# Kernel optimization log

Hardware: AMD Instinct MI355X
Metric: run time of the kernel (lower is better)

## Reference

```python
import jax, jax.numpy as jnp
import numpy as np

EMBED_DIM = 384
NUM_HEADS = 6
HEAD_DIM = EMBED_DIM // NUM_HEADS
MLP_HIDDEN = 4 * EMBED_DIM
LN_EPS = 1e-5


def layer_norm(x, gamma, beta):
    mu = jnp.mean(x, axis=-1, keepdims=True)
    var = jnp.mean((x - mu) ** 2, axis=-1, keepdims=True)
    return (x - mu) * jax.lax.rsqrt(var + LN_EPS) * gamma + beta


def setup_inputs() -> dict:
    key = jax.random.key(0)
    ks = jax.random.split(key, 8)
    D, H = EMBED_DIM, MLP_HIDDEN
    s = 1.0 / np.sqrt(D)
    sh = 1.0 / np.sqrt(H)
    return {
        "x": jax.random.normal(ks[0], (16, 1024, D), dtype=jnp.float32),
        "ln1_g": jnp.ones((D,), jnp.float32),
        "ln1_b": jnp.zeros((D,), jnp.float32),
        "qkv_w": jax.random.uniform(ks[1], (3 * D, D), jnp.float32, -s, s),
        "qkv_b": jax.random.uniform(ks[2], (3 * D,), jnp.float32, -s, s),
        "proj_w": jax.random.uniform(ks[3], (D, D), jnp.float32, -s, s),
        "proj_b": jax.random.uniform(ks[4], (D,), jnp.float32, -s, s),
        "ln2_g": jnp.ones((D,), jnp.float32),
        "ln2_b": jnp.zeros((D,), jnp.float32),
        "fc1_w": jax.random.uniform(ks[5], (H, D), jnp.float32, -s, s),
        "fc1_b": jax.random.uniform(ks[6], (H,), jnp.float32, -s, s),
        "fc2_w": jax.random.uniform(ks[7], (D, H), jnp.float32, -sh, sh),
        "fc2_b": jnp.zeros((D,), jnp.float32),
    }


def reference(x, ln1_g, ln1_b, qkv_w, qkv_b, proj_w, proj_b,
              ln2_g, ln2_b, fc1_w, fc1_b, fc2_w, fc2_b):
    B, N, D = x.shape
    Hh, Dh = NUM_HEADS, HEAD_DIM
    scale = Dh ** -0.5

    # --- attention sublayer (pre-norm) ---
    h = layer_norm(x, ln1_g, ln1_b)
    qkv = h @ qkv_w.T + qkv_b                      # [B,N,3D]
    qkv = qkv.reshape(B, N, 3, Hh, Dh)
    q, k, v = (qkv[:, :, i].transpose(0, 2, 1, 3) for i in range(3))  # [B,H,N,Dh]
    attn = jax.nn.softmax(jnp.einsum('bhnd,bhmd->bhnm', q, k) * scale, axis=-1)
    o = jnp.einsum('bhnm,bhmd->bhnd', attn, v)     # [B,H,N,Dh]
    o = o.transpose(0, 2, 1, 3).reshape(B, N, D)
    x = x + (o @ proj_w.T + proj_b)

    # --- MLP sublayer (pre-norm) ---
    h = layer_norm(x, ln2_g, ln2_b)
    h = jax.nn.gelu(h @ fc1_w.T + fc1_b, approximate=False)
    x = x + (h @ fc2_w.T + fc2_b)
    return x
```

## Files before the change

kernel.cpp:

```cpp
#include <hip/hip_runtime.h>

typedef unsigned short u16;
typedef unsigned int   u32;
typedef __bf16  bf16x8 __attribute__((ext_vector_type(8)));
typedef __bf16  bf16x4_t __attribute__((ext_vector_type(4)));
typedef float   f32x4  __attribute__((ext_vector_type(4)));
typedef float   f32x2  __attribute__((ext_vector_type(2)));

struct Ptrs { const void* p[13]; };

extern "C" __device__ float __ocml_native_exp2_f32(float);

__device__ __forceinline__ float bf2f(u16 u) {
    union { unsigned int i; float f; } c; c.i = ((unsigned int)u) << 16; return c.f;
}
__device__ __forceinline__ u16 f2bf(float f) {
    union { float f; unsigned int i; } c; c.f = f;
    unsigned int u = c.i;
    unsigned int r = (u + 0x7fffu + ((u >> 16) & 1u)) >> 16;
    return (u16)r;
}

__device__ __forceinline__ float wave_sum(float x) {
#pragma unroll
    for (int m = 32; m >= 1; m >>= 1) x += __shfl_xor(x, m);
    return x;
}

__device__ __forceinline__ void g2l16(const u16* g, u16* l) {
    __builtin_amdgcn_global_load_lds(
        (__attribute__((address_space(1))) void*)g,
        (__attribute__((address_space(3))) void*)l, 16, 0, 0);
}

__device__ __forceinline__ int sniff_bf16(const u32* __restrict__ w) {
    int cnt = 0;
    for (int i = 0; i < 32; ++i) {
        u16 lo = (u16)(w[i] & 0xFFFFu);
        int e = (lo >> 7) & 0xFF;
        cnt += (e >= 117 && e <= 123) ? 1 : 0;
    }
    return (cnt >= 16) ? 1 : 0;
}

__global__ __launch_bounds__(256) void k_cvt_ln1(Ptrs ps,
                                                 u16* __restrict__ cw,
                                                 int* __restrict__ flagp,
                                                 u16* __restrict__ cx,
                                                 u16* __restrict__ h)
{
    const int flag = sniff_bf16((const u32*)ps.p[3]);
    if (blockIdx.x == 0 && threadIdx.x == 0) *flagp = flag;

    if (blockIdx.x < 867) {
        const int cum[13] = {0,48,96,55392,55536,73968,74016,74064,74112,
                             147840,148032,221760,221808};
        const int off[12] = {0,384,768,443136,444288,591744,
                             592128,592512,592896,1182720,1184256,1774080};
        int c = blockIdx.x * 256 + threadIdx.x;
        if (c >= 221808) return;
        int seg = 0;
#pragma unroll
        for (int i = 1; i < 12; ++i) seg += (c >= cum[i]) ? 1 : 0;
        int e = (c - cum[seg]) * 8;
        u16* dst = cw + off[seg] + e;
        if (flag) {
            *(uint4*)dst = *((const uint4*)ps.p[seg + 1] + (e >> 3));
        } else {
            const float* s = (const float*)ps.p[seg + 1] + e;
            u16 tmp[8];
#pragma unroll
            for (int t = 0; t < 8; ++t) tmp[t] = f2bf(s[t]);
            *(uint4*)dst = *(const uint4*)tmp;
        }
        return;
    }

    const int wid = threadIdx.x >> 6, lane = threadIdx.x & 63;
    const int row = (blockIdx.x - 867) * 4 + wid;
    const int e0 = lane * 6;
    float v[6]; u16 raw[6];
    float gv[6], bv[6];
    if (flag) {
        const u16* p = (const u16*)ps.p[0] + (size_t)row * 384 + e0;
        u32 w0 = *(const u32*)(p);
        u32 w1 = *(const u32*)(p + 2);
        u32 w2 = *(const u32*)(p + 4);
        raw[0] = (u16)w0; raw[1] = (u16)(w0 >> 16);
        raw[2] = (u16)w1; raw[3] = (u16)(w1 >> 16);
        raw[4] = (u16)w2; raw[5] = (u16)(w2 >> 16);
#pragma unroll
        for (int t = 0; t < 6; t++) v[t] = bf2f(raw[t]);
        const u16* gp = (const u16*)ps.p[1] + e0;
        const u16* bp = (const u16*)ps.p[2] + e0;
#pragma unroll
        for (int t = 0; t < 6; t++) { gv[t] = bf2f(gp[t]); bv[t] = bf2f(bp[t]); }
    } else {
        const float* p = (const float*)ps.p[0] + (size_t)row * 384 + e0;
        f32x2 a0 = *(const f32x2*)(p);
        f32x2 a1 = *(const f32x2*)(p + 2);
        f32x2 a2 = *(const f32x2*)(p + 4);
        v[0] = a0[0]; v[1] = a0[1]; v[2] = a1[0];
        v[3] = a1[1]; v[4] = a2[0]; v[5] = a2[1];
#pragma unroll
        for (int t = 0; t < 6; t++) raw[t] = f2bf(v[t]);
        const float* gp = (const float*)ps.p[1] + e0;
        const float* bp = (const float*)ps.p[2] + e0;
#pragma unroll
        for (int t = 0; t < 6; t++) { gv[t] = gp[t]; bv[t] = bp[t]; }
    }
    u32* pc = (u32*)(cx + (size_t)row * 384 + e0);
    pc[0] = (u32)raw[0] | ((u32)raw[1] << 16);
    pc[1] = (u32)raw[2] | ((u32)raw[3] << 16);
    pc[2] = (u32)raw[4] | ((u32)raw[5] << 16);
    float s = 0.f;
#pragma unroll
    for (int t = 0; t < 6; t++) s += v[t];
    const float mu = wave_sum(s) * (1.0f / 384.0f);
    float vs = 0.f;
#pragma unroll
    for (int t = 0; t < 6; t++) { float d = v[t] - mu; vs += d * d; }
    const float var = wave_sum(vs) * (1.0f / 384.0f);
    const float rs = rsqrtf(var + 1e-5f);
    u16 ow[6];
#pragma unroll
    for (int t = 0; t < 6; t++)
        ow[t] = f2bf((v[t] - mu) * rs * gv[t] + bv[t]);
    u32* po = (u32*)(h + (size_t)row * 384 + e0);
    po[0] = (u32)ow[0] | ((u32)ow[1] << 16);
    po[1] = (u32)ow[2] | ((u32)ow[3] << 16);
    po[2] = (u32)ow[4] | ((u32)ow[5] << 16);
}

template <bool SWAP = false>
__device__ __forceinline__ void gemm_core_128(const u16* __restrict__ A,
                                              const u16* __restrict__ B,
                                              int K, int m0, int n0,
                                              f32x4 (&acc)[4][4])
{
    __shared__ __align__(16) u16 As[128 * 64];
    __shared__ __align__(16) u16 Bs[128 * 64];

    const int tid  = threadIdx.x;
    const int lane = tid & 63;
    const int wid  = tid >> 6;
    const int wm  = (wid >> 1) * 64;
    const int wn  = (wid & 1) * 64;
    const int l15 = lane & 15;
    const int g   = lane >> 4;
    const int srow   = lane >> 3;
    const int schunk = ((lane & 7) ^ srow) * 8;

    const u16* Abase = A + (size_t)(m0 + wid * 32 + srow) * K + schunk;
    const u16* Bbase = B + (size_t)(n0 + wid * 32 + srow) * K + schunk;

    for (int kk = 0; kk < K; kk += 64) {
        __syncthreads();
#pragma unroll
        for (int t = 0; t < 4; ++t) {
            g2l16(Abase + (size_t)t * 8 * K + kk, &As[(wid * 32 + t * 8) * 64]);
            g2l16(Bbase + (size_t)t * 8 * K + kk, &Bs[(wid * 32 + t * 8) * 64]);
        }
        __syncthreads();

#pragma unroll
        for (int ks = 0; ks < 2; ++ks) {
            bf16x8 af[4], bfr[4];
#pragma unroll
            for (int i = 0; i < 4; i++) {
                int row = wm + 16 * i + l15;
                int p = ((ks * 4 + g) ^ (l15 & 7)) * 8;
                af[i] = __builtin_bit_cast(bf16x8,
                         *(const uint4*)&As[row * 64 + p]);
            }
#pragma unroll
            for (int j = 0; j < 4; j++) {
                int row = wn + 16 * j + l15;
                int p = ((ks * 4 + g) ^ (l15 & 7)) * 8;
                bfr[j] = __builtin_bit_cast(bf16x8,
                         *(const uint4*)&Bs[row * 64 + p]);
            }
#pragma unroll
            for (int i = 0; i < 4; i++)
#pragma unroll
                for (int j = 0; j < 4; j++) {
                    if (SWAP)
                        acc[i][j] = __builtin_amdgcn_mfma_f32_16x16x32_bf16(
                                        bfr[j], af[i], acc[i][j], 0, 0, 0);
                    else
                        acc[i][j] = __builtin_amdgcn_mfma_f32_16x16x32_bf16(
                                        af[i], bfr[j], acc[i][j], 0, 0, 0);
                }
        }
    }
}

__device__ __forceinline__ void gemm_core_128x64(const u16* __restrict__ A,
                                                 const u16* __restrict__ B,
                                                 int K, int m0, int n0,
                                                 f32x4 (&acc)[4][2])
{
    __shared__ __align__(16) u16 As[128 * 64];
    __shared__ __align__(16) u16 Bs[64 * 64];

    const int tid  = threadIdx.x;
    const int lane = tid & 63;
    const int wid  = tid >> 6;
    const int wm  = (wid >> 1) * 64;
    const int wn  = (wid & 1) * 32;
    const int l15 = lane & 15;
    const int g   = lane >> 4;
    const int srow   = lane >> 3;
    const int schunk = ((lane & 7) ^ srow) * 8;

    const u16* Abase = A + (size_t)(m0 + wid * 32 + srow) * K + schunk;
    const u16* Bbase = B + (size_t)(n0 + wid * 16 + srow) * K + schunk;

    for (int kk = 0; kk < K; kk += 64) {
        __syncthreads();
#pragma unroll
        for (int t = 0; t < 4; ++t)
            g2l16(Abase + (size_t)t * 8 * K + kk, &As[(wid * 32 + t * 8) * 64]);
#pragma unroll
        for (int t = 0; t < 2; ++t)
            g2l16(Bbase + (size_t)t * 8 * K + kk, &Bs[(wid * 16 + t * 8) * 64]);
        __syncthreads();

#pragma unroll
        for (int ks = 0; ks < 2; ++ks) {
            bf16x8 af[4], bfr[2];
#pragma unroll
            for (int i = 0; i < 4; i++) {
                int row = wm + 16 * i + l15;
                int p = ((ks * 4 + g) ^ (l15 & 7)) * 8;
                af[i] = __builtin_bit_cast(bf16x8,
                         *(const uint4*)&As[row * 64 + p]);
            }
#pragma unroll
            for (int j = 0; j < 2; j++) {
                int row = wn + 16 * j + l15;
                int p = ((ks * 4 + g) ^ (l15 & 7)) * 8;
                bfr[j] = __builtin_bit_cast(bf16x8,
                         *(const uint4*)&Bs[row * 64 + p]);
            }
#pragma unroll
            for (int i = 0; i < 4; i++)
#pragma unroll
                for (int j = 0; j < 2; j++)
                    acc[i][j] = __builtin_amdgcn_mfma_f32_16x16x32_bf16(
                                    af[i], bfr[j], acc[i][j], 0, 0, 0);
        }
    }
}

__global__ __launch_bounds__(256) void k_layernorm(const u16* __restrict__ in,
                                                   const u16* __restrict__ g,
                                                   const u16* __restrict__ b,
                                                   u16* __restrict__ out,
                                                   int nrows)
{
    const int wid = threadIdx.x >> 6, lane = threadIdx.x & 63;
    const int row = blockIdx.x * 4 + wid;
    if (row >= nrows) return;
    const int e0 = lane * 6;
    float v[6];
    const u16* p = in + (size_t)row * 384 + e0;
    u32 w0 = *(const u32*)(p);
    u32 w1 = *(const u32*)(p + 2);
    u32 w2 = *(const u32*)(p + 4);
    v[0] = bf2f((u16)w0); v[1] = bf2f((u16)(w0 >> 16));
    v[2] = bf2f((u16)w1); v[3] = bf2f((u16)(w1 >> 16));
    v[4] = bf2f((u16)w2); v[5] = bf2f((u16)(w2 >> 16));
    float s = 0.f;
#pragma unroll
    for (int t = 0; t < 6; t++) s += v[t];
    const float mu = wave_sum(s) * (1.0f / 384.0f);
    float vs = 0.f;
#pragma unroll
    for (int t = 0; t < 6; t++) { float d = v[t] - mu; vs += d * d; }
    const float var = wave_sum(vs) * (1.0f / 384.0f);
    const float rs = rsqrtf(var + 1e-5f);
    const u32* gg = (const u32*)(g + e0);
    const u32* bb = (const u32*)(b + e0);
    u32 gw[3] = {gg[0], gg[1], gg[2]};
    u32 bw[3] = {bb[0], bb[1], bb[2]};
    u16 ow[6];
#pragma unroll
    for (int t = 0; t < 6; t++) {
        u16 ge = (u16)(gw[t >> 1] >> ((t & 1) * 16));
        u16 be = (u16)(bw[t >> 1] >> ((t & 1) * 16));
        ow[t] = f2bf((v[t] - mu) * rs * bf2f(ge) + bf2f(be));
    }
    u32* po = (u32*)(out + (size_t)row * 384 + e0);
    po[0] = (u32)ow[0] | ((u32)ow[1] << 16);
    po[1] = (u32)ow[2] | ((u32)ow[3] << 16);
    po[2] = (u32)ow[4] | ((u32)ow[5] << 16);
}

__global__ __launch_bounds__(256) void k_gemm_qkv(const u16* __restrict__ A,
                                                  const u16* __restrict__ W,
                                                  const u16* __restrict__ bias,
                                                  u16* __restrict__ q,
                                                  u16* __restrict__ kbuf,
                                                  u16* __restrict__ vT)
{
    const int id = blockIdx.x, slot = id & 7, idx = id >> 3;
    const int m0 = (slot * 16 + idx / 9) * 128;
    const int n0 = (idx % 9) * 128;
    f32x4 acc[4][4];
#pragma unroll
    for (int i = 0; i < 4; i++)
#pragma unroll
        for (int j = 0; j < 4; j++) acc[i][j] = f32x4{0.f, 0.f, 0.f, 0.f};
    gemm_core_128<true>(A, W, 384, m0, n0, acc);
    const int lane = threadIdx.x & 63, wid = threadIdx.x >> 6;
    const int wm = (wid >> 1) * 64, wn = (wid & 1) * 64;
    const int l15 = lane & 15, rq = (lane >> 4) * 4;
#pragma unroll
    for (int i = 0; i < 4; i++) {
        const int gr = m0 + wm + 16 * i + l15;
        const int bb = gr >> 10, nn = gr & 1023;
#pragma unroll
        for (int j = 0; j < 4; j++) {
            const int gcb = n0 + wn + 16 * j + rq;
            const int part = gcb / 384, rem = gcb % 384;
            const int head = rem >> 6, dhb = rem & 63;
            const int bh = bb * 6 + head;
            float vals[4];
#pragma unroll
            for (int r = 0; r < 4; r++) vals[r] = acc[i][j][r] + bf2f(bias[gcb + r]);
            if (part == 2) {
#pragma unroll
                for (int r = 0; r < 4; r++)
                    vT[((size_t)bh * 64 + dhb + r) * 1024 + nn] = f2bf(vals[r]);
            } else {
                u16* dst = part ? kbuf : q;
                u32 lo = (u32)f2bf(vals[0]) | ((u32)f2bf(vals[1]) << 16);
                u32 hi = (u32)f2bf(vals[2]) | ((u32)f2bf(vals[3]) << 16);
                uint2 pk; pk.x = lo; pk.y = hi;
                *(uint2*)&dst[((size_t)bh * 1024 + nn) * 64 + dhb] = pk;
            }
        }
    }
}

__global__ __launch_bounds__(256) void k_attn(const u16* __restrict__ q,
                                              const u16* __restrict__ kk,
                                              const u16* __restrict__ vT,
                                              u16* __restrict__ o)
{
    __shared__ __align__(16) u16 Ks[128 * 64];
    __shared__ __align__(16) u16 Vs[2][64 * 64];
    __shared__ __align__(16) u16 Ps[128 * 64];

    const int tid = threadIdx.x, lane = tid & 63, wid = tid >> 6;
    const int l15 = lane & 15, g = lane >> 4, q8 = g * 8;
    const int id = blockIdx.x;
    const int bh = (id & 7) * 12 + ((id >> 3) >> 3);
    const int q0 = ((id >> 3) & 7) * 128;
    const int wrow = wid * 32;

    const u16* Q = q  + (size_t)bh * 65536;
    const u16* K = kk + (size_t)bh * 65536;
    const u16* V = vT + (size_t)bh * 65536;

    const int srow   = lane >> 3;
    const int schunk = ((lane & 7) ^ srow) * 8;
    const int rd0 = ((0 + g) ^ (l15 & 7)) * 8;
    const int rd1 = ((4 + g) ^ (l15 & 7)) * 8;
    int pcol[4];
#pragma unroll
    for (int ip = 0; ip < 4; ++ip)
        pcol[ip] = (((ip * 2 + (g >> 1)) ^ (l15 & 7)) * 8) + (g & 1) * 4;

    bf16x8 aq[2][2];
#pragma unroll
    for (int jp = 0; jp < 2; ++jp)
#pragma unroll
        for (int ks = 0; ks < 2; ++ks) {
            bf16x8 t = __builtin_bit_cast(bf16x8,
                *(const uint4*)&Q[(size_t)(q0 + wrow + jp * 16 + l15) * 64
                                  + ks * 32 + q8]);
#pragma unroll
            for (int e = 0; e < 8; ++e)
                t[e] = (__bf16)((float)t[e] * 0.18033688f);
            aq[jp][ks] = t;
        }

    f32x4 ob[2][4];
#pragma unroll
    for (int i = 0; i < 2; ++i)
#pragma unroll
        for (int j = 0; j < 4; ++j) ob[i][j] = f32x4{0.f, 0.f, 0.f, 0.f};
    float lsum[2] = {0.f, 0.f};

    for (int kt2 = 0; kt2 < 8; ++kt2) {
        __syncthreads();
#pragma unroll
        for (int t = 0; t < 4; ++t) {
            int r0 = wid * 32 + t * 8;
            g2l16(&K[(size_t)(kt2 * 128 + r0 + srow) * 64 + schunk], &Ks[r0 * 64]);
        }
#pragma unroll
        for (int h = 0; h < 2; ++h)
#pragma unroll
            for (int t = 0; t < 2; ++t) {
                int r0 = wid * 16 + t * 8;
                g2l16(&V[(size_t)(r0 + srow) * 1024 + kt2 * 128 + h * 64 + schunk],
                      &Vs[h][r0 * 64]);
            }
        __syncthreads();

#pragma unroll 1
        for (int h = 0; h < 2; ++h) {
            f32x4 st[4][2];
#pragma unroll
            for (int ip = 0; ip < 4; ++ip)
#pragma unroll
                for (int jp = 0; jp < 2; ++jp) st[ip][jp] = f32x4{0.f,0.f,0.f,0.f};
            __builtin_amdgcn_s_setprio(1);
#pragma unroll
            for (int ip = 0; ip < 4; ++ip) {
                int rbase = (h * 64 + ip * 16 + l15) * 64;
                bf16x8 bk0 = __builtin_bit_cast(bf16x8,
                    *(const uint4*)&Ks[rbase + rd0]);
                bf16x8 bk1 = __builtin_bit_cast(bf16x8,
                    *(const uint4*)&Ks[rbase + rd1]);
#pragma unroll
                for (int jp = 0; jp < 2; ++jp) {
                    st[ip][jp] = __builtin_amdgcn_mfma_f32_16x16x32_bf16(
                                    bk0, aq[jp][0], st[ip][jp], 0, 0, 0);
                    st[ip][jp] = __builtin_amdgcn_mfma_f32_16x16x32_bf16(
                                    bk1, aq[jp][1], st[ip][jp], 0, 0, 0);
                }
            }
            __builtin_amdgcn_s_setprio(0);

#pragma unroll
            for (int jp = 0; jp < 2; ++jp) {
                float ps = 0.f;
#pragma unroll
                for (int ip = 0; ip < 4; ++ip)
#pragma unroll
                    for (int r = 0; r < 4; ++r) {
                        float p = __ocml_native_exp2_f32(st[ip][jp][r]);
                        st[ip][jp][r] = p;
                        ps += p;
                    }
                lsum[jp] += ps;
            }

#pragma unroll
            for (int ip = 0; ip < 4; ++ip)
#pragma unroll
                for (int jp = 0; jp < 2; ++jp) {
                    bf16x4_t pk;
#pragma unroll
                    for (int r = 0; r < 4; ++r) pk[r] = (__bf16)st[ip][jp][r];
                    *(bf16x4_t*)&Ps[(wrow + jp*16 + l15) * 64 + pcol[ip]] = pk;
                }

            __builtin_amdgcn_s_setprio(1);
#pragma unroll
            for (int ks = 0; ks < 2; ++ks) {
                const int rdo = ks ? rd1 : rd0;
                bf16x8 ap[2];
#pragma unroll
                for (int i = 0; i < 2; ++i)
                    ap[i] = __builtin_bit_cast(bf16x8,
                        *(const uint4*)&Ps[(wrow + i*16 + l15) * 64 + rdo]);
#pragma unroll
                for (int jv = 0; jv < 4; ++jv) {
                    bf16x8 bv = __builtin_bit_cast(bf16x8,
                        *(const uint4*)&Vs[h][(jv * 16 + l15) * 64 + rdo]);
#pragma unroll
                    for (int i = 0; i < 2; ++i)
                        ob[i][jv] = __builtin_amdgcn_mfma_f32_16x16x32_bf16(
                                      ap[i], bv, ob[i][jv], 0, 0, 0);
                }
            }
            __builtin_amdgcn_s_setprio(0);
        }
    }

#pragma unroll
    for (int jp = 0; jp < 2; ++jp) {
        lsum[jp] += __shfl_xor(lsum[jp], 16);
        lsum[jp] += __shfl_xor(lsum[jp], 32);
    }
    const int bb = bh / 6, hh = bh % 6;
#pragma unroll
    for (int i = 0; i < 2; ++i)
#pragma unroll
        for (int r = 0; r < 4; ++r) {
            int src = (lane & 48) | (g * 4 + r);
            float linv = 1.0f / __shfl(lsum[i], src);
            int row = q0 + wrow + i * 16 + g * 4 + r;
#pragma unroll
            for (int jv = 0; jv < 4; ++jv) {
                int dh = jv * 16 + l15;
                o[((size_t)(bb * 1024 + row)) * 384 + hh * 64 + dh] =
                    f2bf(ob[i][jv][r] * linv);
            }
        }
}

__global__ __launch_bounds__(256) void k_gemm_proj(const u16* __restrict__ A,
                                                   const u16* __restrict__ W,
                                                   const u16* __restrict__ bias,
                                                   const u16* __restrict__ xin,
                                                   u16* __restrict__ x1)
{
    const int id = blockIdx.x, slot = id & 7, idx = id >> 3;
    const int m0 = (slot * 16 + idx / 6) * 128;
    const int n0 = (idx % 6) * 64;
    f32x4 acc[4][2];
#pragma unroll
    for (int i = 0; i < 4; i++)
#pragma unroll
        for (int j = 0; j < 2; j++) acc[i][j] = f32x4{0.f, 0.f, 0.f, 0.f};
    gemm_core_128x64(A, W, 384, m0, n0, acc);
    const int lane = threadIdx.x & 63, wid = threadIdx.x >> 6;
    const int wm = (wid >> 1) * 64, wn = (wid & 1) * 32;
    const int l15 = lane & 15, rq = (lane >> 4) * 4;
#pragma unroll
    for (int i = 0; i < 4; i++)
#pragma unroll
        for (int j = 0; j < 2; j++)
#pragma unroll
            for (int r = 0; r < 4; r++) {
                int gr = m0 + wm + 16 * i + rq + r;
                int gc = n0 + wn + 16 * j + l15;
                size_t ix = (size_t)gr * 384 + gc;
                x1[ix] = f2bf(acc[i][j][r] + bf2f(bias[gc]) + bf2f(xin[ix]));
            }
}

__global__ __launch_bounds__(256) void k_gemm_fc1(const u16* __restrict__ A,
                                                  const u16* __restrict__ W,
                                                  const u16* __restrict__ bias,
                                                  u16* __restrict__ hmid)
{
    const int id = blockIdx.x, slot = id & 7, idx = id >> 3;
    const int mbase = (slot * 8 + idx / 12) * 256;
    const int n0 = (idx % 12) * 128;
#pragma unroll 1
    for (int sub = 0; sub < 2; ++sub) {
        const int m0 = mbase + sub * 128;
        f32x4 acc[4][4];
#pragma unroll
        for (int i = 0; i < 4; i++)
#pragma unroll
            for (int j = 0; j < 4; j++) acc[i][j] = f32x4{0.f, 0.f, 0.f, 0.f};
        gemm_core_128(A, W, 384, m0, n0, acc);
        const int lane = threadIdx.x & 63, wid = threadIdx.x >> 6;
        const int wm = (wid >> 1) * 64, wn = (wid & 1) * 64;
        const int l15 = lane & 15, rq = (lane >> 4) * 4;
#pragma unroll
        for (int i = 0; i < 4; i++)
#pragma unroll
            for (int j = 0; j < 4; j++)
#pragma unroll
                for (int r = 0; r < 4; r++) {
                    int gr = m0 + wm + 16 * i + rq + r;
                    int gc = n0 + wn + 16 * j + l15;
                    float v = acc[i][j][r] + bf2f(bias[gc]);
                    float u2 = v * (2.3022084f + 0.1029433f * v * v);
                    float ge = v * __builtin_amdgcn_rcpf(
                                   1.0f + __ocml_native_exp2_f32(-u2));
                    hmid[(size_t)gr * 1536 + gc] = f2bf(ge);
                }
    }
}

__global__ __launch_bounds__(256) void k_gemm_fc2(const u16* __restrict__ A,
                                                  const u16* __restrict__ W,
                                                  const u16* __restrict__ bias,
                                                  const u16* __restrict__ x1,
                                                  void* __restrict__ outv,
                                                  const int* __restrict__ flagp)
{
    const int id = blockIdx.x, slot = id & 7, idx = id >> 3;
    const int m0 = (slot * 16 + idx / 6) * 128;
    const int n0 = (idx % 6) * 64;
    f32x4 acc[4][2];
#pragma unroll
    for (int i = 0; i < 4; i++)
#pragma unroll
        for (int j = 0; j < 2; j++) acc[i][j] = f32x4{0.f, 0.f, 0.f, 0.f};
    gemm_core_128x64(A, W, 1536, m0, n0, acc);
    const int lane = threadIdx.x & 63, wid = threadIdx.x >> 6;
    const int wm = (wid >> 1) * 64, wn = (wid & 1) * 32;
    const int l15 = lane & 15, rq = (lane >> 4) * 4;
    const int isbf = *flagp;
    u16*   ob = (u16*)outv;
    float* of = (float*)outv;
#pragma unroll
    for (int i = 0; i < 4; i++)
#pragma unroll
        for (int j = 0; j < 2; j++)
#pragma unroll
            for (int r = 0; r < 4; r++) {
                int gr = m0 + wm + 16 * i + rq + r;
                int gc = n0 + wn + 16 * j + l15;
                size_t ix = (size_t)gr * 384 + gc;
                float v = acc[i][j][r] + bf2f(bias[gc]) + bf2f(x1[ix]);
                if (isbf) ob[ix] = f2bf(v);
                else      of[ix] = v;
            }
}

extern "C" void kernel_launch(void* const* d_in, const int* in_sizes, int n_in,
                              void* d_out, int out_size, void* d_ws, size_t ws_size,
                              hipStream_t stream)
{
    char* ws = (char*)d_ws;
    u16*   cw   = (u16*)(ws + 0);
    int*   flag = (int*)(ws + 3548928);
    u16*   cx   = (u16*)(ws + 3549184);
    u16*   h    = (u16*)(ws + 16132096);
    u16*   x1   = (u16*)(ws + 28715008);
    u16*   q    = (u16*)(ws + 53880832);
    u16*   kbuf = (u16*)(ws + 66463744);
    u16*   vT   = (u16*)(ws + 79046656);
    u16*   o    = (u16*)(ws + 91629568);
    u16*   hmid = (u16*)(ws + 53880832);

    const u16* c_qkv_w  = cw + 768;
    const u16* c_qkv_b  = cw + 443136;
    const u16* c_proj_w = cw + 444288;
    const u16* c_proj_b = cw + 591744;
    const u16* c_ln2_g  = cw + 592128;
    const u16* c_ln2_b  = cw + 592512;
    const u16* c_fc1_w  = cw + 592896;
    const u16* c_fc1_b  = cw + 1182720;
    const u16* c_fc2_w  = cw + 1184256;
    const u16* c_fc2_b  = cw + 1774080;

    Ptrs ps;
    for (int i = 0; i < 13; ++i) ps.p[i] = d_in[i];

    k_cvt_ln1<<<4963, 256, 0, stream>>>(ps, cw, flag, cx, h);
    k_gemm_qkv<<<1152, 256, 0, stream>>>(h, c_qkv_w, c_qkv_b, q, kbuf, vT);
    k_attn<<<768, 256, 0, stream>>>(q, kbuf, vT, o);
    k_gemm_proj<<<768, 256, 0, stream>>>(o, c_proj_w, c_proj_b, cx, x1);
    k_layernorm<<<4096, 256, 0, stream>>>(x1, c_ln2_g, c_ln2_b, h, 16384);
    k_gemm_fc1<<<768, 256, 0, stream>>>(h, c_fc1_w, c_fc1_b, hmid);
    k_gemm_fc2<<<768, 256, 0, stream>>>(hmid, c_fc2_w, c_fc2_b, x1,
                                        d_out, flag);
    (void)in_sizes; (void)n_in; (void)out_size; (void)ws_size; (void)c_fc2_b;
}
```

Baseline: 259.9 us.

## Fold LayerNorm affine and normalization into GEMM epilogues via per-row stats

Instead of materializing normalized LayerNorm outputs, the kernels fold gamma into the qkv and fc1 weights, precompute per-column gamma·W and beta·W+bias sums, and store only per-row rstd and -mu·rstd. The GEMMs then consume the raw bf16 input (cx or x1) and apply row scale and offset in the epilogue. This removes writing and re-reading the normalized activation tensors, at the cost of extra per-element epilogue loads and a precision change, since the GEMM now runs on un-centered raw inputs.

```diff
diff --git a/kernel.cpp b/kernel.cpp
--- a/kernel.cpp
+++ b/kernel.cpp
@@ -47,7 +47,12 @@
                                                  u16* __restrict__ cw,
                                                  int* __restrict__ flagp,
                                                  u16* __restrict__ cx,
-                                                 u16* __restrict__ h)
+                                                 float* __restrict__ rs1,
+                                                 float* __restrict__ mrs1,
+                                                 float* __restrict__ Gq,
+                                                 float* __restrict__ Bq,
+                                                 float* __restrict__ Gf,
+                                                 float* __restrict__ Bf)
 {
     const int flag = sniff_bf16((const u32*)ps.p[3]);
     if (blockIdx.x == 0 && threadIdx.x == 0) *flagp = flag;
@@ -64,14 +69,83 @@
         for (int i = 1; i < 12; ++i) seg += (c >= cum[i]) ? 1 : 0;
         int e = (c - cum[seg]) * 8;
         u16* dst = cw + off[seg] + e;
+        const bool scale = (seg == 2) || (seg == 8);
+        float gvv[8];
+        if (scale) {
+            const int k0 = e % 384;
+            const void* gp = (seg == 2) ? ps.p[1] : ps.p[7];
+            if (flag) {
+                const u16* g16 = (const u16*)gp + k0;
+#pragma unroll
+                for (int t = 0; t < 8; ++t) gvv[t] = bf2f(g16[t]);
+            } else {
+                const float* g32 = (const float*)gp + k0;
+#pragma unroll
+                for (int t = 0; t < 8; ++t) gvv[t] = g32[t];
+            }
+        }
         if (flag) {
-            *(uint4*)dst = *((const uint4*)ps.p[seg + 1] + (e >> 3));
+            uint4 wv = *((const uint4*)ps.p[seg + 1] + (e >> 3));
+            if (!scale) { *(uint4*)dst = wv; }
+            else {
+                u16 src[8]; *(uint4*)src = wv;
+                u16 tmp[8];
+#pragma unroll
+                for (int t = 0; t < 8; ++t) tmp[t] = f2bf(bf2f(src[t]) * gvv[t]);
+                *(uint4*)dst = *(const uint4*)tmp;
+            }
         } else {
             const float* s = (const float*)ps.p[seg + 1] + e;
             u16 tmp[8];
 #pragma unroll
-            for (int t = 0; t < 8; ++t) tmp[t] = f2bf(s[t]);
+            for (int t = 0; t < 8; ++t) {
+                float x = s[t];
+                if (scale) x *= gvv[t];
+                tmp[t] = f2bf(x);
+            }
             *(uint4*)dst = *(const uint4*)tmp;
+        }
+        return;
+    }
+
+    if (blockIdx.x >= 4963) {
+        const int wid = threadIdx.x >> 6, lane = threadIdx.x & 63;
+        const int col = (blockIdx.x - 4963) * 4 + wid;
+        if (col >= 2688) return;
+        const void *W, *Gm, *Bt, *bias; float *Gd, *Bd; int c;
+        if (col < 1152) { c = col;        W = ps.p[3]; Gm = ps.p[1];
+                          Bt = ps.p[2];   bias = ps.p[4]; Gd = Gq; Bd = Bq; }
+        else            { c = col - 1152; W = ps.p[9]; Gm = ps.p[7];
+                          Bt = ps.p[8];   bias = ps.p[10]; Gd = Gf; Bd = Bf; }
+        const int e0 = lane * 6;
+        float gs = 0.f, bs = 0.f;
+        if (flag) {
+            const u16* wp = (const u16*)W + (size_t)c * 384 + e0;
+            const u16* gp = (const u16*)Gm + e0;
+            const u16* bp = (const u16*)Bt + e0;
+#pragma unroll
+            for (int t = 0; t < 6; ++t) {
+                float w = bf2f(wp[t]);
+                gs += w * bf2f(gp[t]);
+                bs += w * bf2f(bp[t]);
+            }
+        } else {
+            const float* wp = (const float*)W + (size_t)c * 384 + e0;
+            const float* gp = (const float*)Gm + e0;
+            const float* bp = (const float*)Bt + e0;
+#pragma unroll
+            for (int t = 0; t < 6; ++t) {
+                float w = wp[t];
+                gs += w * gp[t];
+                bs += w * bp[t];
+            }
+        }
+        gs = wave_sum(gs); bs = wave_sum(bs);
+        if (lane == 0) {
+            float bi = flag ? bf2f(((const u16*)bias)[c])
+                            : ((const float*)bias)[c];
+            Gd[c] = gs;
+            Bd[c] = bs + bi;
         }
         return;
     }
@@ -80,7 +154,6 @@
     const int row = (blockIdx.x - 867) * 4 + wid;
     const int e0 = lane * 6;
     float v[6]; u16 raw[6];
-    float gv[6], bv[6];
     if (flag) {
         const u16* p = (const u16*)ps.p[0] + (size_t)row * 384 + e0;
         u32 w0 = *(const u32*)(p);
@@ -91,10 +164,6 @@
         raw[4] = (u16)w2; raw[5] = (u16)(w2 >> 16);
 #pragma unroll
         for (int t = 0; t < 6; t++) v[t] = bf2f(raw[t]);
-        const u16* gp = (const u16*)ps.p[1] + e0;
-        const u16* bp = (const u16*)ps.p[2] + e0;
-#pragma unroll
-        for (int t = 0; t < 6; t++) { gv[t] = bf2f(gp[t]); bv[t] = bf2f(bp[t]); }
     } else {
         const float* p = (const float*)ps.p[0] + (size_t)row * 384 + e0;
         f32x2 a0 = *(const f32x2*)(p);
@@ -104,10 +173,6 @@
         v[3] = a1[1]; v[4] = a2[0]; v[5] = a2[1];
 #pragma unroll
         for (int t = 0; t < 6; t++) raw[t] = f2bf(v[t]);
-        const float* gp = (const float*)ps.p[1] + e0;
-        const float* bp = (const float*)ps.p[2] + e0;
-#pragma unroll
-        for (int t = 0; t < 6; t++) { gv[t] = gp[t]; bv[t] = bp[t]; }
     }
     u32* pc = (u32*)(cx + (size_t)row * 384 + e0);
     pc[0] = (u32)raw[0] | ((u32)raw[1] << 16);
@@ -122,14 +187,34 @@
     for (int t = 0; t < 6; t++) { float d = v[t] - mu; vs += d * d; }
     const float var = wave_sum(vs) * (1.0f / 384.0f);
     const float rs = rsqrtf(var + 1e-5f);
-    u16 ow[6];
-#pragma unroll
-    for (int t = 0; t < 6; t++)
-        ow[t] = f2bf((v[t] - mu) * rs * gv[t] + bv[t]);
-    u32* po = (u32*)(h + (size_t)row * 384 + e0);
-    po[0] = (u32)ow[0] | ((u32)ow[1] << 16);
-    po[1] = (u32)ow[2] | ((u32)ow[3] << 16);
-    po[2] = (u32)ow[4] | ((u32)ow[5] << 16);
+    if (lane == 0) { rs1[row] = rs; mrs1[row] = -mu * rs; }
+}
+
+__global__ __launch_bounds__(256) void k_stats2(const u16* __restrict__ in,
+                                                float* __restrict__ rs2,
+                                                float* __restrict__ mrs2)
+{
+    const int wid = threadIdx.x >> 6, lane = threadIdx.x & 63;
+    const int row = blockIdx.x * 4 + wid;
+    const int e0 = lane * 6;
+    const u16* p = in + (size_t)row * 384 + e0;
+    u32 w0 = *(const u32*)(p);
+    u32 w1 = *(const u32*)(p + 2);
+    u32 w2 = *(const u32*)(p + 4);
+    float v[6];
+    v[0] = bf2f((u16)w0); v[1] = bf2f((u16)(w0 >> 16));
+    v[2] = bf2f((u16)w1); v[3] = bf2f((u16)(w1 >> 16));
+    v[4] = bf2f((u16)w2); v[5] = bf2f((u16)(w2 >> 16));
+    float s = 0.f;
+#pragma unroll
+    for (int t = 0; t < 6; t++) s += v[t];
+    const float mu = wave_sum(s) * (1.0f / 384.0f);
+    float vs = 0.f;
+#pragma unroll
+    for (int t = 0; t < 6; t++) { float d = v[t] - mu; vs += d * d; }
+    const float var = wave_sum(vs) * (1.0f / 384.0f);
+    const float rs = rsqrtf(var + 1e-5f);
+    if (lane == 0) { rs2[row] = rs; mrs2[row] = -mu * rs; }
 }
 
 template <bool SWAP = false>
@@ -253,53 +338,12 @@
     }
 }
 
-__global__ __launch_bounds__(256) void k_layernorm(const u16* __restrict__ in,
-                                                   const u16* __restrict__ g,
-                                                   const u16* __restrict__ b,
-                                                   u16* __restrict__ out,
-                                                   int nrows)
-{
-    const int wid = threadIdx.x >> 6, lane = threadIdx.x & 63;
-    const int row = blockIdx.x * 4 + wid;
-    if (row >= nrows) return;
-    const int e0 = lane * 6;
-    float v[6];
-    const u16* p = in + (size_t)row * 384 + e0;
-    u32 w0 = *(const u32*)(p);
-    u32 w1 = *(const u32*)(p + 2);
-    u32 w2 = *(const u32*)(p + 4);
-    v[0] = bf2f((u16)w0); v[1] = bf2f((u16)(w0 >> 16));
-    v[2] = bf2f((u16)w1); v[3] = bf2f((u16)(w1 >> 16));
-    v[4] = bf2f((u16)w2); v[5] = bf2f((u16)(w2 >> 16));
-    float s = 0.f;
-#pragma unroll
-    for (int t = 0; t < 6; t++) s += v[t];
-    const float mu = wave_sum(s) * (1.0f / 384.0f);
-    float vs = 0.f;
-#pragma unroll
-    for (int t = 0; t < 6; t++) { float d = v[t] - mu; vs += d * d; }
-    const float var = wave_sum(vs) * (1.0f / 384.0f);
-    const float rs = rsqrtf(var + 1e-5f);
-    const u32* gg = (const u32*)(g + e0);
-    const u32* bb = (const u32*)(b + e0);
-    u32 gw[3] = {gg[0], gg[1], gg[2]};
-    u32 bw[3] = {bb[0], bb[1], bb[2]};
-    u16 ow[6];
-#pragma unroll
-    for (int t = 0; t < 6; t++) {
-        u16 ge = (u16)(gw[t >> 1] >> ((t & 1) * 16));
-        u16 be = (u16)(bw[t >> 1] >> ((t & 1) * 16));
-        ow[t] = f2bf((v[t] - mu) * rs * bf2f(ge) + bf2f(be));
-    }
-    u32* po = (u32*)(out + (size_t)row * 384 + e0);
-    po[0] = (u32)ow[0] | ((u32)ow[1] << 16);
-    po[1] = (u32)ow[2] | ((u32)ow[3] << 16);
-    po[2] = (u32)ow[4] | ((u32)ow[5] << 16);
-}
-
 __global__ __launch_bounds__(256) void k_gemm_qkv(const u16* __restrict__ A,
                                                   const u16* __restrict__ W,
-                                                  const u16* __restrict__ bias,
+                                                  const float* __restrict__ rs1,
+                                                  const float* __restrict__ mrs1,
+                                                  const float* __restrict__ Gq,
+                                                  const float* __restrict__ Bq,
                                                   u16* __restrict__ q,
                                                   u16* __restrict__ kbuf,
                                                   u16* __restrict__ vT)
@@ -320,6 +364,7 @@
     for (int i = 0; i < 4; i++) {
         const int gr = m0 + wm + 16 * i + l15;
         const int bb = gr >> 10, nn = gr & 1023;
+        const float r1 = rs1[gr], m1 = mrs1[gr];
 #pragma unroll
         for (int j = 0; j < 4; j++) {
             const int gcb = n0 + wn + 16 * j + rq;
@@ -328,7 +373,8 @@
             const int bh = bb * 6 + head;
             float vals[4];
 #pragma unroll
-            for (int r = 0; r < 4; r++) vals[r] = acc[i][j][r] + bf2f(bias[gcb + r]);
+            for (int r = 0; r < 4; r++)
+                vals[r] = acc[i][j][r] * r1 + m1 * Gq[gcb + r] + Bq[gcb + r];
             if (part == 2) {
 #pragma unroll
                 for (int r = 0; r < 4; r++)
@@ -538,7 +584,10 @@
 
 __global__ __launch_bounds__(256) void k_gemm_fc1(const u16* __restrict__ A,
                                                   const u16* __restrict__ W,
-                                                  const u16* __restrict__ bias,
+                                                  const float* __restrict__ rs2,
+                                                  const float* __restrict__ mrs2,
+                                                  const float* __restrict__ Gf,
+                                                  const float* __restrict__ Bf,
                                                   u16* __restrict__ hmid)
 {
     const int id = blockIdx.x, slot = id & 7, idx = id >> 3;
@@ -564,7 +613,7 @@
                 for (int r = 0; r < 4; r++) {
                     int gr = m0 + wm + 16 * i + rq + r;
                     int gc = n0 + wn + 16 * j + l15;
-                    float v = acc[i][j][r] + bf2f(bias[gc]);
+                    float v = acc[i][j][r] * rs2[gr] + mrs2[gr] * Gf[gc] + Bf[gc];
                     float u2 = v * (2.3022084f + 0.1029433f * v * v);
                     float ge = v * __builtin_amdgcn_rcpf(
                                    1.0f + __ocml_native_exp2_f32(-u2));
@@ -618,35 +667,40 @@
     u16*   cw   = (u16*)(ws + 0);
     int*   flag = (int*)(ws + 3548928);
     u16*   cx   = (u16*)(ws + 3549184);
-    u16*   h    = (u16*)(ws + 16132096);
     u16*   x1   = (u16*)(ws + 28715008);
     u16*   q    = (u16*)(ws + 53880832);
     u16*   kbuf = (u16*)(ws + 66463744);
     u16*   vT   = (u16*)(ws + 79046656);
     u16*   o    = (u16*)(ws + 91629568);
     u16*   hmid = (u16*)(ws + 53880832);
+    float* rs1  = (float*)(ws + 104212480);
+    float* mrs1 = (float*)(ws + 104278016);
+    float* rs2  = (float*)(ws + 104343552);
+    float* mrs2 = (float*)(ws + 104409088);
+    float* Gq   = (float*)(ws + 104474624);
+    float* Bq   = (float*)(ws + 104479232);
+    float* Gf   = (float*)(ws + 104483840);
+    float* Bf   = (float*)(ws + 104489984);
 
     const u16* c_qkv_w  = cw + 768;
-    const u16* c_qkv_b  = cw + 443136;
     const u16* c_proj_w = cw + 444288;
     const u16* c_proj_b = cw + 591744;
-    const u16* c_ln2_g  = cw + 592128;
-    const u16* c_ln2_b  = cw + 592512;
     const u16* c_fc1_w  = cw + 592896;
-    const u16* c_fc1_b  = cw + 1182720;
     const u16* c_fc2_w  = cw + 1184256;
     const u16* c_fc2_b  = cw + 1774080;
 
     Ptrs ps;
     for (int i = 0; i < 13; ++i) ps.p[i] = d_in[i];
 
-    k_cvt_ln1<<<4963, 256, 0, stream>>>(ps, cw, flag, cx, h);
-    k_gemm_qkv<<<1152, 256, 0, stream>>>(h, c_qkv_w, c_qkv_b, q, kbuf, vT);
+    k_cvt_ln1<<<5635, 256, 0, stream>>>(ps, cw, flag, cx,
+                                        rs1, mrs1, Gq, Bq, Gf, Bf);
+    k_gemm_qkv<<<1152, 256, 0, stream>>>(cx, c_qkv_w, rs1, mrs1, Gq, Bq,
+                                         q, kbuf, vT);
     k_attn<<<768, 256, 0, stream>>>(q, kbuf, vT, o);
     k_gemm_proj<<<768, 256, 0, stream>>>(o, c_proj_w, c_proj_b, cx, x1);
-    k_layernorm<<<4096, 256, 0, stream>>>(x1, c_ln2_g, c_ln2_b, h, 16384);
-    k_gemm_fc1<<<768, 256, 0, stream>>>(h, c_fc1_w, c_fc1_b, hmid);
+    k_stats2<<<4096, 256, 0, stream>>>(x1, rs2, mrs2);
+    k_gemm_fc1<<<768, 256, 0, stream>>>(x1, c_fc1_w, rs2, mrs2, Gf, Bf, hmid);
     k_gemm_fc2<<<768, 256, 0, stream>>>(hmid, c_fc2_w, c_fc2_b, x1,
                                         d_out, flag);
-    (void)in_sizes; (void)n_in; (void)out_size; (void)ws_size; (void)c_fc2_b;
-}
+    (void)in_sizes; (void)n_in; (void)out_size; (void)ws_size;
+}
```

Result: slower. 282.0 us (+8.5%).

## Split attention block across eight waves with sixteen query rows each

Applied to the files above, without the earlier changes.

The attention kernel now launches 512 threads per block instead of 256. Each of the eight waves owns 16 query rows rather than 32, and the K/V tile loads are redistributed across the extra waves. This halves per-wave accumulator and score registers, which should allow more waves in flight to hide LDS and MFMA latency. In exchange each wave re-reads the same K and V fragments from LDS for half the MFMA work, so LDS read traffic per FLOP doubles.

```diff
diff --git a/kernel.cpp b/kernel.cpp
--- a/kernel.cpp
+++ b/kernel.cpp
@@ -344,7 +344,7 @@
     }
 }
 
-__global__ __launch_bounds__(256) void k_attn(const u16* __restrict__ q,
+__global__ __launch_bounds__(512) void k_attn(const u16* __restrict__ q,
                                               const u16* __restrict__ kk,
                                               const u16* __restrict__ vT,
                                               u16* __restrict__ o)
@@ -358,7 +358,7 @@
     const int id = blockIdx.x;
     const int bh = (id & 7) * 12 + ((id >> 3) >> 3);
     const int q0 = ((id >> 3) & 7) * 128;
-    const int wrow = wid * 32;
+    const int wrow = wid * 16;
 
     const u16* Q = q  + (size_t)bh * 65536;
     const u16* K = kk + (size_t)bh * 65536;
@@ -373,51 +373,42 @@
     for (int ip = 0; ip < 4; ++ip)
         pcol[ip] = (((ip * 2 + (g >> 1)) ^ (l15 & 7)) * 8) + (g & 1) * 4;
 
-    bf16x8 aq[2][2];
-#pragma unroll
-    for (int jp = 0; jp < 2; ++jp)
-#pragma unroll
-        for (int ks = 0; ks < 2; ++ks) {
-            bf16x8 t = __builtin_bit_cast(bf16x8,
-                *(const uint4*)&Q[(size_t)(q0 + wrow + jp * 16 + l15) * 64
-                                  + ks * 32 + q8]);
-#pragma unroll
-            for (int e = 0; e < 8; ++e)
-                t[e] = (__bf16)((float)t[e] * 0.18033688f);
-            aq[jp][ks] = t;
-        }
-
-    f32x4 ob[2][4];
-#pragma unroll
-    for (int i = 0; i < 2; ++i)
-#pragma unroll
-        for (int j = 0; j < 4; ++j) ob[i][j] = f32x4{0.f, 0.f, 0.f, 0.f};
-    float lsum[2] = {0.f, 0.f};
+    bf16x8 aq[2];
+#pragma unroll
+    for (int ks = 0; ks < 2; ++ks) {
+        bf16x8 t = __builtin_bit_cast(bf16x8,
+            *(const uint4*)&Q[(size_t)(q0 + wrow + l15) * 64 + ks * 32 + q8]);
+#pragma unroll
+        for (int e = 0; e < 8; ++e)
+            t[e] = (__bf16)((float)t[e] * 0.18033688f);
+        aq[ks] = t;
+    }
+
+    f32x4 ob[4];
+#pragma unroll
+    for (int j = 0; j < 4; ++j) ob[j] = f32x4{0.f, 0.f, 0.f, 0.f};
+    float lsum = 0.f;
 
     for (int kt2 = 0; kt2 < 8; ++kt2) {
         __syncthreads();
 #pragma unroll
-        for (int t = 0; t < 4; ++t) {
-            int r0 = wid * 32 + t * 8;
+        for (int t = 0; t < 2; ++t) {
+            int r0 = wid * 16 + t * 8;
             g2l16(&K[(size_t)(kt2 * 128 + r0 + srow) * 64 + schunk], &Ks[r0 * 64]);
         }
 #pragma unroll
-        for (int h = 0; h < 2; ++h)
-#pragma unroll
-            for (int t = 0; t < 2; ++t) {
-                int r0 = wid * 16 + t * 8;
-                g2l16(&V[(size_t)(r0 + srow) * 1024 + kt2 * 128 + h * 64 + schunk],
-                      &Vs[h][r0 * 64]);
-            }
+        for (int h = 0; h < 2; ++h) {
+            int r0 = wid * 8;
+            g2l16(&V[(size_t)(r0 + srow) * 1024 + kt2 * 128 + h * 64 + schunk],
+                  &Vs[h][r0 * 64]);
+        }
         __syncthreads();
 
 #pragma unroll 1
         for (int h = 0; h < 2; ++h) {
-            f32x4 st[4][2];
-#pragma unroll
-            for (int ip = 0; ip < 4; ++ip)
-#pragma unroll
-                for (int jp = 0; jp < 2; ++jp) st[ip][jp] = f32x4{0.f,0.f,0.f,0.f};
+            f32x4 st[4];
+#pragma unroll
+            for (int ip = 0; ip < 4; ++ip) st[ip] = f32x4{0.f, 0.f, 0.f, 0.f};
             __builtin_amdgcn_s_setprio(1);
 #pragma unroll
             for (int ip = 0; ip < 4; ++ip) {
@@ -426,83 +417,65 @@
                     *(const uint4*)&Ks[rbase + rd0]);
                 bf16x8 bk1 = __builtin_bit_cast(bf16x8,
                     *(const uint4*)&Ks[rbase + rd1]);
-#pragma unroll
-                for (int jp = 0; jp < 2; ++jp) {
-                    st[ip][jp] = __builtin_amdgcn_mfma_f32_16x16x32_bf16(
-                                    bk0, aq[jp][0], st[ip][jp], 0, 0, 0);
-                    st[ip][jp] = __builtin_amdgcn_mfma_f32_16x16x32_bf16(
-                                    bk1, aq[jp][1], st[ip][jp], 0, 0, 0);
+                st[ip] = __builtin_amdgcn_mfma_f32_16x16x32_bf16(
+                            bk0, aq[0], st[ip], 0, 0, 0);
+                st[ip] = __builtin_amdgcn_mfma_f32_16x16x32_bf16(
+                            bk1, aq[1], st[ip], 0, 0, 0);
+            }
+            __builtin_amdgcn_s_setprio(0);
+
+            float ps = 0.f;
+#pragma unroll
+            for (int ip = 0; ip < 4; ++ip)
+#pragma unroll
+                for (int r = 0; r < 4; ++r) {
+                    float p = __ocml_native_exp2_f32(st[ip][r]);
+                    st[ip][r] = p;
+                    ps += p;
                 }
-            }
-            __builtin_amdgcn_s_setprio(0);
-
-#pragma unroll
-            for (int jp = 0; jp < 2; ++jp) {
-                float ps = 0.f;
-#pragma unroll
-                for (int ip = 0; ip < 4; ++ip)
-#pragma unroll
-                    for (int r = 0; r < 4; ++r) {
-                        float p = __ocml_native_exp2_f32(st[ip][jp][r]);
-                        st[ip][jp][r] = p;
-                        ps += p;
-                    }
-                lsum[jp] += ps;
-            }
-
-#pragma unroll
-            for (int ip = 0; ip < 4; ++ip)
-#pragma unroll
-                for (int jp = 0; jp < 2; ++jp) {
-                    bf16x4_t pk;
-#pragma unroll
-                    for (int r = 0; r < 4; ++r) pk[r] = (__bf16)st[ip][jp][r];
-                    *(bf16x4_t*)&Ps[(wrow + jp*16 + l15) * 64 + pcol[ip]] = pk;
-                }
+            lsum += ps;
+
+#pragma unroll
+            for (int ip = 0; ip < 4; ++ip) {
+                bf16x4_t pk;
+#pragma unroll
+                for (int r = 0; r < 4; ++r) pk[r] = (__bf16)st[ip][r];
+                *(bf16x4_t*)&Ps[(wrow + l15) * 64 + pcol[ip]] = pk;
+            }
 
             __builtin_amdgcn_s_setprio(1);
 #pragma unroll
             for (int ks = 0; ks < 2; ++ks) {
                 const int rdo = ks ? rd1 : rd0;
-                bf16x8 ap[2];
-#pragma unroll
-                for (int i = 0; i < 2; ++i)
-                    ap[i] = __builtin_bit_cast(bf16x8,
-                        *(const uint4*)&Ps[(wrow + i*16 + l15) * 64 + rdo]);
+                bf16x8 ap = __builtin_bit_cast(bf16x8,
+                    *(const uint4*)&Ps[(wrow + l15) * 64 + rdo]);
 #pragma unroll
                 for (int jv = 0; jv < 4; ++jv) {
                     bf16x8 bv = __builtin_bit_cast(bf16x8,
                         *(const uint4*)&Vs[h][(jv * 16 + l15) * 64 + rdo]);
-#pragma unroll
-                    for (int i = 0; i < 2; ++i)
-                        ob[i][jv] = __builtin_amdgcn_mfma_f32_16x16x32_bf16(
-                                      ap[i], bv, ob[i][jv], 0, 0, 0);
+                    ob[jv] = __builtin_amdgcn_mfma_f32_16x16x32_bf16(
+                                ap, bv, ob[jv], 0, 0, 0);
                 }
             }
             __builtin_amdgcn_s_setprio(0);
         }
     }
 
-#pragma unroll
-    for (int jp = 0; jp < 2; ++jp) {
-        lsum[jp] += __shfl_xor(lsum[jp], 16);
-        lsum[jp] += __shfl_xor(lsum[jp], 32);
-    }
+    lsum += __shfl_xor(lsum, 16);
+    lsum += __shfl_xor(lsum, 32);
     const int bb = bh / 6, hh = bh % 6;
 #pragma unroll
-    for (int i = 0; i < 2; ++i)
-#pragma unroll
-        for (int r = 0; r < 4; ++r) {
-            int src = (lane & 48) | (g * 4 + r);
-            float linv = 1.0f / __shfl(lsum[i], src);
-            int row = q0 + wrow + i * 16 + g * 4 + r;
-#pragma unroll
-            for (int jv = 0; jv < 4; ++jv) {
-                int dh = jv * 16 + l15;
-                o[((size_t)(bb * 1024 + row)) * 384 + hh * 64 + dh] =
-                    f2bf(ob[i][jv][r] * linv);
-            }
-        }
+    for (int r = 0; r < 4; ++r) {
+        int src = (lane & 48) | (g * 4 + r);
+        float linv = 1.0f / __shfl(lsum, src);
+        int row = q0 + wrow + g * 4 + r;
+#pragma unroll
+        for (int jv = 0; jv < 4; ++jv) {
+            int dh = jv * 16 + l15;
+            o[((size_t)(bb * 1024 + row)) * 384 + hh * 64 + dh] =
+                f2bf(ob[jv][r] * linv);
+        }
+    }
 }
 
 __global__ __launch_bounds__(256) void k_gemm_proj(const u16* __restrict__ A,
@@ -642,7 +615,7 @@
 
     k_cvt_ln1<<<4963, 256, 0, stream>>>(ps, cw, flag, cx, h);
     k_gemm_qkv<<<1152, 256, 0, stream>>>(h, c_qkv_w, c_qkv_b, q, kbuf, vT);
-    k_attn<<<768, 256, 0, stream>>>(q, kbuf, vT, o);
+    k_attn<<<768, 512, 0, stream>>>(q, kbuf, vT, o);
     k_gemm_proj<<<768, 256, 0, stream>>>(o, c_proj_w, c_proj_b, cx, x1);
     k_layernorm<<<4096, 256, 0, stream>>>(x1, c_ln2_g, c_ln2_b, h, 16384);
     k_gemm_fc1<<<768, 256, 0, stream>>>(h, c_fc1_w, c_fc1_b, hmid);
```

Result: faster. 254.6 us (-2.1%).
